# Optimization experiments

Hardware: AMD Instinct MI355X
Metric: run time of the kernel (lower is better)

## Reference

```python
import jax, jax.numpy as jnp
import numpy as np

N = 50000   # nodes
E = 800000  # edges
F = 2       # num_feats
D = 2       # output_dim
H = 64      # hidden_size
L = 2       # num_layers
T = 12      # seq_len
HZN = 12    # horizon
NEG_SLOPE = 0.2


def setup_inputs() -> dict:
    key = jax.random.key(0)
    ks = jax.random.split(key, 10)
    x = jax.random.normal(ks[0], (T, N, F), dtype=jnp.float32)
    src = jax.random.randint(ks[1], (E,), 0, N, dtype=jnp.int32)
    dst = jax.random.randint(ks[2], (E,), 0, N, dtype=jnp.int32)

    def conv_params(k, fin):
        k1, k2, k3 = jax.random.split(k, 3)
        s = 1.0 / np.sqrt(fin)
        W = (jax.random.normal(k1, (3, fin, H), jnp.float32) * s)
        al = (jax.random.normal(k2, (3, H), jnp.float32) * s)
        ar = (jax.random.normal(k3, (3, H), jnp.float32) * s)
        b = jnp.zeros((3, H), jnp.float32)
        return W, al, ar, b

    enc_W0, enc_al0, enc_ar0, enc_b0 = conv_params(ks[3], F + H)
    enc_W1, enc_al1, enc_ar1, enc_b1 = conv_params(ks[4], 2 * H)
    dec_W0, dec_al0, dec_ar0, dec_b0 = conv_params(ks[5], D + H)
    dec_W1, dec_al1, dec_ar1, dec_b1 = conv_params(ks[6], 2 * H)
    proj_W = jax.random.normal(ks[7], (H, D), jnp.float32) / np.sqrt(H)
    proj_b = jnp.zeros((D,), jnp.float32)
    return dict(x=x, src=src, dst=dst,
                enc_W0=enc_W0, enc_al0=enc_al0, enc_ar0=enc_ar0, enc_b0=enc_b0,
                enc_W1=enc_W1, enc_al1=enc_al1, enc_ar1=enc_ar1, enc_b1=enc_b1,
                dec_W0=dec_W0, dec_al0=dec_al0, dec_ar0=dec_ar0, dec_b0=dec_b0,
                dec_W1=dec_W1, dec_al1=dec_al1, dec_ar1=dec_ar1, dec_b1=dec_b1,
                proj_W=proj_W, proj_b=proj_b)


def _gat(feat, W, al, ar, b, src, dst):
    # DGL GATConv, single head: fc -> edge attention -> edge softmax -> aggregate.
    h = feat @ W                              # [N, H]
    el = (h * al).sum(-1)                     # [N] source attention logits
    er = (h * ar).sum(-1)                     # [N] destination attention logits
    e = jax.nn.leaky_relu(el[src] + er[dst], NEG_SLOPE)   # [E]
    m = jax.ops.segment_max(e, dst, num_segments=N)       # per-dst max (stable softmax)
    ex = jnp.exp(e - m[dst])                               # [E]
    s = jax.ops.segment_sum(ex, dst, num_segments=N)       # [N]
    alpha = ex / jnp.maximum(s[dst], 1e-9)                 # [E] edge softmax
    out = jax.ops.segment_sum(h[src] * alpha[:, None], dst, num_segments=N)  # [N, H]
    return out + b


def _gru(xin, hx, W, al, ar, b, src, dst):
    iv = jnp.concatenate([xin, hx], axis=1)
    r = jax.nn.sigmoid(_gat(iv, W[0], al[0], ar[0], b[0], src, dst))
    z = jax.nn.sigmoid(_gat(iv, W[1], al[1], ar[1], b[1], src, dst))
    hc = jnp.tanh(_gat(jnp.concatenate([xin, r * hx], axis=1), W[2], al[2], ar[2], b[2], src, dst))
    return z * hx + (1.0 - z) * hc


def reference(x, src, dst,
              enc_W0, enc_al0, enc_ar0, enc_b0,
              enc_W1, enc_al1, enc_ar1, enc_b1,
              dec_W0, dec_al0, dec_ar0, dec_b0,
              dec_W1, dec_al1, dec_ar1, dec_b1,
              proj_W, proj_b):
    enc_params = [(enc_W0, enc_al0, enc_ar0, enc_b0), (enc_W1, enc_al1, enc_ar1, enc_b1)]
    dec_params = [(dec_W0, dec_al0, dec_ar0, dec_b0), (dec_W1, dec_al1, dec_ar1, dec_b1)]

    def enc_step(hstack, xt):
        out = xt
        new = []
        for i, (W, al, ar, b) in enumerate(enc_params):
            hn = _gru(out, hstack[i], W, al, ar, b, src, dst)
            new.append(hn)
            out = hn
        return jnp.stack(new), None

    h0 = jnp.zeros((L, N, H), x.dtype)
    hT, _ = jax.lax.scan(enc_step, h0, x)

    def dec_step(carry, _):
        dec_in, hstack = carry
        out = dec_in
        new = []
        for i, (W, al, ar, b) in enumerate(dec_params):
            hn = _gru(out, hstack[i], W, al, ar, b, src, dst)
            new.append(hn)
            out = hn
        pred = out @ proj_W + proj_b                 # [N, D]
        return (pred, jnp.stack(new)), pred

    dec_in0 = jnp.zeros((N, D), x.dtype)
    _, outputs = jax.lax.scan(dec_step, (dec_in0, hT), None, length=HZN)
    return outputs  # [horizon, N, output_dim]
```

## Files before the change

kernel.cpp:

```cpp
#include <hip/hip_runtime.h>
#include <hip/hip_bf16.h>

__device__ __forceinline__ float wsum64(float v) {
#pragma unroll
  for (int m = 32; m > 0; m >>= 1) v += __shfl_xor(v, m, 64);
  return v;
}
__device__ __forceinline__ float gsum16(float v) {
#pragma unroll
  for (int m = 8; m > 0; m >>= 1) v += __shfl_xor(v, m, 16);
  return v;
}
__device__ __forceinline__ float lrelu(float x) { return x > 0.f ? x : 0.2f * x; }
__device__ __forceinline__ float sigf(float x) { return 1.f / (1.f + __expf(-x)); }
__device__ __forceinline__ float dp4(float4 a, float4 b) {
  return a.x * b.x + a.y * b.y + a.z * b.z + a.w * b.w;
}

#define MM1(f, row)                                        \
  {                                                        \
    float4 w_ = W4[(row) * 16 + l16];                      \
    acc.x = fmaf((f), w_.x, acc.x);                        \
    acc.y = fmaf((f), w_.y, acc.y);                        \
    acc.z = fmaf((f), w_.z, acc.z);                        \
    acc.w = fmaf((f), w_.w, acc.w);                        \
  }

__global__ void hist_k(const int* __restrict__ dst, int* __restrict__ cnt, int e) {
  int i = blockIdx.x * blockDim.x + threadIdx.x;
  if (i < e) atomicAdd(&cnt[dst[i]], 1);
}

__global__ __launch_bounds__(256) void bsum_k(const int* __restrict__ cnt,
                                              int* __restrict__ bsum, int n) {
  __shared__ int red[4];
  int base = blockIdx.x * 1024;
  int t = threadIdx.x;
  int v = 0;
#pragma unroll
  for (int i = 0; i < 4; i++) {
    int idx = base + t + i * 256;
    v += (idx < n) ? cnt[idx] : 0;
  }
#pragma unroll
  for (int m = 32; m > 0; m >>= 1) v += __shfl_xor(v, m, 64);
  if ((t & 63) == 0) red[t >> 6] = v;
  __syncthreads();
  if (t == 0) bsum[blockIdx.x] = red[0] + red[1] + red[2] + red[3];
}

__global__ __launch_bounds__(1024) void scan_bsum_k(int* __restrict__ bsum,
                                                    int* __restrict__ rpn, int nb) {
  __shared__ int buf[1024];
  int t = threadIdx.x;
  int v = (t < nb) ? bsum[t] : 0;
  buf[t] = v;
  __syncthreads();
  int val = v;
  for (int off = 1; off < 1024; off <<= 1) {
    int u = (t >= off) ? buf[t - off] : 0;
    __syncthreads();
    val += u;
    buf[t] = val;
    __syncthreads();
  }
  if (t < nb) bsum[t] = val - v;
  if (t == nb - 1) *rpn = val;
}

__global__ __launch_bounds__(1024) void scan_fin_k(const int* __restrict__ cnt,
                                                   const int* __restrict__ bsum,
                                                   int* __restrict__ rp,
                                                   int* __restrict__ cursor, int n) {
  __shared__ int buf[1024];
  int t = threadIdx.x;
  int idx = blockIdx.x * 1024 + t;
  int v = (idx < n) ? cnt[idx] : 0;
  buf[t] = v;
  __syncthreads();
  int val = v;
  for (int off = 1; off < 1024; off <<= 1) {
    int u = (t >= off) ? buf[t - off] : 0;
    __syncthreads();
    val += u;
    buf[t] = val;
    __syncthreads();
  }
  if (idx < n) {
    int e = bsum[blockIdx.x] + val - v;
    rp[idx] = e;
    cursor[idx] = e;
  }
}

__global__ void scatter_k(const int* __restrict__ src, const int* __restrict__ dst,
                          int* __restrict__ cursor, int* __restrict__ srcs, int e) {
  int i = blockIdx.x * blockDim.x + threadIdx.x;
  if (i < e) {
    int pos = atomicAdd(&cursor[dst[i]], 1);
    srcs[pos] = src[i];
  }
}

template <int FA>
__global__ __launch_bounds__(512) void mm_k(
    const float* __restrict__ xa, const float* __restrict__ xb,
    const float* __restrict__ Wg, const float* __restrict__ al, const float* __restrict__ ar,
    float* __restrict__ hb, float* __restrict__ el, float* __restrict__ er, int n) {
  constexpr int KP = FA + 64;
  __shared__ float Wl[KP * 128];
  __shared__ float Xl[32 * KP];
  for (int i = threadIdx.x; i < KP * 64; i += 512) {
    float2 wv = {Wg[i], Wg[(size_t)KP * 64 + i]};
    *(float2*)&Wl[i * 2] = wv;
  }
  int rbase = blockIdx.x * 32;
  for (int i = threadIdx.x; i < 32 * KP; i += 512) {
    int row = i / KP, k = i - row * KP;
    int r = rbase + row; if (r >= n) r = n - 1;
    Xl[i] = (k < FA) ? xa[(size_t)r * FA + k] : xb[(size_t)r * 64 + (k - FA)];
  }
  __syncthreads();
  int lane = threadIdx.x & 63, w = threadIdx.x >> 6;
  int rb = rbase + w * 4;
  if (rb >= n) return;
  float alr = al[lane], arr_ = ar[lane];
  float alz = al[64 + lane], arz = ar[64 + lane];
  float accr[4], accz[4];
#pragma unroll
  for (int i = 0; i < 4; i++) { accr[i] = 0.f; accz[i] = 0.f; }
  const int xoff = (w * 4) * KP;
#pragma unroll 8
  for (int k = 0; k < KP; k += 2) {
    float2 w0 = *(const float2*)&Wl[(k * 64 + lane) * 2];
    float2 w1 = *(const float2*)&Wl[((k + 1) * 64 + lane) * 2];
#pragma unroll
    for (int i = 0; i < 4; i++) {
      float2 xv = *(const float2*)&Xl[xoff + i * KP + k];
      accr[i] = fmaf(xv.x, w0.x, accr[i]);
      accz[i] = fmaf(xv.x, w0.y, accz[i]);
      accr[i] = fmaf(xv.y, w1.x, accr[i]);
      accz[i] = fmaf(xv.y, w1.y, accz[i]);
    }
  }
#pragma unroll
  for (int i = 0; i < 4; i++) {
    int r = rb + i;
    bool ok = r < n;
    if (ok) {
      hb[(size_t)r * 128 + lane] = accr[i];
      hb[(size_t)r * 128 + 64 + lane] = accz[i];
    }
    float s0 = wsum64(accr[i] * alr);
    float s1 = wsum64(accz[i] * alz);
    float s2 = wsum64(accr[i] * arr_);
    float s3 = wsum64(accz[i] * arz);
    if (ok && lane == 0) {
      el[(size_t)r * 2 + 0] = s0;
      el[(size_t)r * 2 + 1] = s1;
      er[(size_t)r * 2 + 0] = s2;
      er[(size_t)r * 2 + 1] = s3;
    }
  }
}

template <int FA>
__global__ __launch_bounds__(512) void kb_k(
    const int* __restrict__ rp, const int* __restrict__ srcs,
    const float* __restrict__ hbuf, const float* __restrict__ elrz,
    const float* __restrict__ errz, const float* __restrict__ b,
    const float* __restrict__ xa, const float* __restrict__ hx,
    const float* __restrict__ Wc, const float* __restrict__ alc,
    const float* __restrict__ arc,
    float* __restrict__ hc, float* __restrict__ elc, float* __restrict__ erc,
    float* __restrict__ zb, int n) {
  constexpr int KP = FA + 64;
  __shared__ float WlC[KP * 64];
  for (int i = threadIdx.x; i < KP * 64; i += 512) {
    int k = i >> 6, c = i & 63;
    int ks = (k < 64) ? (FA + k) : (k - 64);
    WlC[i] = Wc[(size_t)ks * 64 + c];
  }
  __syncthreads();
  int l16 = threadIdx.x & 15;
  int d = blockIdx.x * 32 + (threadIdx.x >> 4);
  if (d >= n) return;
  int beg = rp[d], deg = rp[d + 1] - beg;
  float2 erd = ((const float2*)errz)[d];
  const float4* h4 = (const float4*)hbuf;
  float4 accr = {0, 0, 0, 0}, accz = {0, 0, 0, 0};
  float sr = 0.f, sz = 0.f;
  for (int base = 0; base < deg; base += 16) {
    int k = base + l16;
    int s = 0;
    float exr = 0.f, exz = 0.f;
    if (k < deg) {
      s = srcs[beg + k];
      float2 el = ((const float2*)elrz)[s];
      exr = __expf(lrelu(el.x + erd.x));
      exz = __expf(lrelu(el.y + erd.y));
      sr += exr; sz += exz;
    }
#pragma unroll
    for (int j = 0; j < 16; j++) {
      int sj = __shfl(s, j, 16);
      float aj = __shfl(exr, j, 16);
      float zj = __shfl(exz, j, 16);
      float4 hr = h4[(size_t)sj * 32 + l16];
      float4 hz = h4[(size_t)sj * 32 + 16 + l16];
      accr.x = fmaf(aj, hr.x, accr.x); accr.y = fmaf(aj, hr.y, accr.y);
      accr.z = fmaf(aj, hr.z, accr.z); accr.w = fmaf(aj, hr.w, accr.w);
      accz.x = fmaf(zj, hz.x, accz.x); accz.y = fmaf(zj, hz.y, accz.y);
      accz.z = fmaf(zj, hz.z, accz.z); accz.w = fmaf(zj, hz.w, accz.w);
    }
  }
  sr = gsum16(sr); sz = gsum16(sz);
  float invr = 1.f / fmaxf(sr, 1e-9f);
  float invz = 1.f / fmaxf(sz, 1e-9f);
  float4 br4 = ((const float4*)b)[l16];
  float4 bz4 = ((const float4*)(b + 64))[l16];
  float4 hx4 = ((const float4*)hx)[(size_t)d * 16 + l16];
  float4 rv, zv;
  rv.x = sigf(fmaf(accr.x, invr, br4.x)) * hx4.x;
  rv.y = sigf(fmaf(accr.y, invr, br4.y)) * hx4.y;
  rv.z = sigf(fmaf(accr.z, invr, br4.z)) * hx4.z;
  rv.w = sigf(fmaf(accr.w, invr, br4.w)) * hx4.w;
  zv.x = sigf(fmaf(accz.x, invz, bz4.x));
  zv.y = sigf(fmaf(accz.y, invz, bz4.y));
  zv.z = sigf(fmaf(accz.z, invz, bz4.z));
  zv.w = sigf(fmaf(accz.w, invz, bz4.w));
  ((float4*)zb)[(size_t)d * 16 + l16] = zv;
  const float4* W4 = (const float4*)WlC;
  float4 acc = {0, 0, 0, 0};
#pragma unroll
  for (int o = 0; o < 16; o++) {
    float f0 = __shfl(rv.x, o, 16);
    float f1 = __shfl(rv.y, o, 16);
    float f2 = __shfl(rv.z, o, 16);
    float f3 = __shfl(rv.w, o, 16);
    MM1(f0, 4 * o + 0); MM1(f1, 4 * o + 1);
    MM1(f2, 4 * o + 2); MM1(f3, 4 * o + 3);
  }
  if (FA == 2) {
    float f0 = xa[(size_t)d * 2 + 0];
    float f1 = xa[(size_t)d * 2 + 1];
    MM1(f0, 64); MM1(f1, 65);
  } else {
    float4 xv = ((const float4*)xa)[(size_t)d * 16 + l16];
#pragma unroll
    for (int o = 0; o < 16; o++) {
      float f0 = __shfl(xv.x, o, 16);
      float f1 = __shfl(xv.y, o, 16);
      float f2 = __shfl(xv.z, o, 16);
      float f3 = __shfl(xv.w, o, 16);
      MM1(f0, 64 + 4 * o + 0); MM1(f1, 64 + 4 * o + 1);
      MM1(f2, 64 + 4 * o + 2); MM1(f3, 64 + 4 * o + 3);
    }
  }
  float4 alv = ((const float4*)alc)[l16];
  float4 arv = ((const float4*)arc)[l16];
  float sl = gsum16(dp4(acc, alv));
  float sr2 = gsum16(dp4(acc, arv));
  if (l16 == 0) { elc[d] = sl; erc[d] = sr2; }
  ((float4*)hc)[(size_t)d * 16 + l16] = acc;
}

__global__ __launch_bounds__(512) void kc_k(
    const int* __restrict__ rp, const int* __restrict__ srcs,
    const float* __restrict__ hc, const float* __restrict__ elc,
    const float* __restrict__ erc, const float* __restrict__ bc,
    const float* __restrict__ zb, float* __restrict__ hstate,
    const float* __restrict__ projW, const float* __restrict__ projb,
    float* __restrict__ outp, int n) {
  int l16 = threadIdx.x & 15;
  int d = blockIdx.x * 32 + (threadIdx.x >> 4);
  if (d >= n) return;
  int beg = rp[d], deg = rp[d + 1] - beg;
  float erd = erc[d];
  const float4* h4 = (const float4*)hc;
  float4 acg = {0, 0, 0, 0};
  float ssum = 0.f;
  for (int base0 = 0; base0 < deg; base0 += 16) {
    int k = base0 + l16;
    int s = 0;
    float ex = 0.f;
    if (k < deg) {
      s = srcs[beg + k];
      ex = __expf(lrelu(elc[s] + erd));
      ssum += ex;
    }
#pragma unroll
    for (int j = 0; j < 16; j++) {
      int sj = __shfl(s, j, 16);
      float aj = __shfl(ex, j, 16);
      float4 hv = h4[(size_t)sj * 16 + l16];
      acg.x = fmaf(aj, hv.x, acg.x); acg.y = fmaf(aj, hv.y, acg.y);
      acg.z = fmaf(aj, hv.z, acg.z); acg.w = fmaf(aj, hv.w, acg.w);
    }
  }
  ssum = gsum16(ssum);
  float inv = 1.f / fmaxf(ssum, 1e-9f);
  float4 bc4 = ((const float4*)bc)[l16];
  float4 z4 = ((const float4*)zb)[(size_t)d * 16 + l16];
  float4 hx4 = ((const float4*)hstate)[(size_t)d * 16 + l16];
  float4 hcv, hn;
  hcv.x = tanhf(fmaf(acg.x, inv, bc4.x));
  hcv.y = tanhf(fmaf(acg.y, inv, bc4.y));
  hcv.z = tanhf(fmaf(acg.z, inv, bc4.z));
  hcv.w = tanhf(fmaf(acg.w, inv, bc4.w));
  hn.x = z4.x * hx4.x + (1.f - z4.x) * hcv.x;
  hn.y = z4.y * hx4.y + (1.f - z4.y) * hcv.y;
  hn.z = z4.z * hx4.z + (1.f - z4.z) * hcv.z;
  hn.w = z4.w * hx4.w + (1.f - z4.w) * hcv.w;
  ((float4*)hstate)[(size_t)d * 16 + l16] = hn;
  if (outp) {
    const float4* wp4 = (const float4*)projW;
    float4 a0p = wp4[l16 * 2], a1p = wp4[l16 * 2 + 1];
    float p0 = gsum16(hn.x * a0p.x + hn.y * a0p.z + hn.z * a1p.x + hn.w * a1p.z) + projb[0];
    float p1 = gsum16(hn.x * a0p.y + hn.y * a0p.w + hn.z * a1p.y + hn.w * a1p.w) + projb[1];
    if (l16 == 0) {
      outp[(size_t)d * 2 + 0] = p0;
      outp[(size_t)d * 2 + 1] = p1;
    }
  }
}

extern "C" void kernel_launch(void* const* d_in, const int* in_sizes, int n_in,
                              void* d_out, int out_size, void* d_ws, size_t ws_size,
                              hipStream_t stream) {
  const int T = 12, F = 2, H = 64;
  const float* x = (const float*)d_in[0];
  const int* src = (const int*)d_in[1];
  const int* dst = (const int*)d_in[2];
  const float* Ws[4] = {(const float*)d_in[3], (const float*)d_in[7],
                        (const float*)d_in[11], (const float*)d_in[15]};
  const float* als[4] = {(const float*)d_in[4], (const float*)d_in[8],
                         (const float*)d_in[12], (const float*)d_in[16]};
  const float* ars[4] = {(const float*)d_in[5], (const float*)d_in[9],
                         (const float*)d_in[13], (const float*)d_in[17]};
  const float* bs[4] = {(const float*)d_in[6], (const float*)d_in[10],
                        (const float*)d_in[14], (const float*)d_in[18]};
  const float* proj_W = (const float*)d_in[19];
  const float* proj_b = (const float*)d_in[20];
  float* out = (float*)d_out;

  const int E = in_sizes[1];
  const int N = in_sizes[0] / (T * F);
  const int NB = (N + 1023) / 1024;

  char* wp = (char*)d_ws;
  size_t off = 0;
  auto carve = [&](size_t bytes) {
    void* p = wp + off;
    off = (off + bytes + 255) & ~(size_t)255;
    return p;
  };
  int* counts = (int*)carve((size_t)N * 4);
  int* bsum = (int*)carve((size_t)NB * 4);
  int* rp = (int*)carve((size_t)(N + 1) * 4);
  int* cursor = (int*)carve((size_t)N * 4);
  int* srcs = (int*)carve((size_t)E * 4);
  float* hs0 = (float*)carve((size_t)N * H * 4);
  float* hs1 = (float*)carve((size_t)N * H * 4);
  float* hbuf = (float*)carve((size_t)N * 2 * H * 4);
  float* elrz = (float*)carve((size_t)N * 2 * 4);
  float* errz = (float*)carve((size_t)N * 2 * 4);
  float* hcb = (float*)carve((size_t)N * H * 4);
  float* elc = (float*)carve((size_t)N * 4);
  float* erc = (float*)carve((size_t)N * 4);
  float* zbuf = (float*)carve((size_t)N * H * 4);
  float* zero2 = (float*)carve((size_t)N * F * 4);
  (void)ws_size;

  const int G_E = (E + 255) / 256;
  const int G32 = (N + 31) / 32;

  hipMemsetAsync(counts, 0, (size_t)N * 4, stream);
  hist_k<<<G_E, 256, 0, stream>>>(dst, counts, E);
  bsum_k<<<NB, 256, 0, stream>>>(counts, bsum, N);
  scan_bsum_k<<<1, 1024, 0, stream>>>(bsum, rp + N, NB);
  scan_fin_k<<<NB, 1024, 0, stream>>>(counts, bsum, rp, cursor, N);
  scatter_k<<<G_E, 256, 0, stream>>>(src, dst, cursor, srcs, E);

  hipMemsetAsync(hs0, 0, (size_t)N * H * 4, stream);
  hipMemsetAsync(hs1, 0, (size_t)N * H * 4, stream);
  hipMemsetAsync(zero2, 0, (size_t)N * F * 4, stream);

  for (int i = 0; i < 48; i++) {
    bool enc = i < 24;
    int j = enc ? i : i - 24;
    int t = j >> 1, layer = j & 1;
    int type = (enc ? 0 : 2) + layer;
    const float* W = Ws[type];
    const float* al = als[type];
    const float* ar = ars[type];
    const float* b = bs[type];
    int FA = layer ? 64 : 2;
    size_t KP = FA + 64;
    const float* Wc = W + (size_t)2 * KP * 64;
    const float* xa = layer ? hs0
                            : (enc ? x + (size_t)t * N * 2
                                   : (t == 0 ? zero2 : out + (size_t)(t - 1) * N * 2));
    float* hstate = layer ? hs1 : hs0;
    float* outp = (!enc && layer) ? out + (size_t)t * N * 2 : nullptr;

    if (FA == 2) {
      mm_k<2><<<G32, 512, 0, stream>>>(xa, hstate, W, al, ar, hbuf, elrz, errz, N);
      kb_k<2><<<G32, 512, 0, stream>>>(rp, srcs, hbuf, elrz, errz, b, xa, hstate,
                                       Wc, al + 128, ar + 128, hcb, elc, erc, zbuf, N);
    } else {
      mm_k<64><<<G32, 512, 0, stream>>>(xa, hstate, W, al, ar, hbuf, elrz, errz, N);
      kb_k<64><<<G32, 512, 0, stream>>>(rp, srcs, hbuf, elrz, errz, b, xa, hstate,
                                        Wc, al + 128, ar + 128, hcb, elc, erc, zbuf, N);
    }
    kc_k<<<G32, 512, 0, stream>>>(rp, srcs, hcb, elc, erc, b + 128, zbuf, hstate,
                                  proj_W, proj_b, outp, N);
  }
  (void)out_size; (void)n_in;
}
```

Before: 7.665 ms.

## Wavefront-pipeline encoder layers by merging layer-1 step t with layer-0 step t+1

The encoder is reordered so that layer 1 at time t and layer 0 at time t+1 run together. Their attention-aggregation and GRU-update kernels are merged into single launches with twice the grid, and block index picks which cell a block serves. A second set of scratch buffers keeps the two cells' intermediates separate. The goal is fewer serialized launches and more blocks in flight per launch. In exchange, the merged kernels always reserve the larger 128x64 shared tile, and the pipelined path only runs when the workspace is big enough.

```diff
diff --git a/kernel.cpp b/kernel.cpp
--- a/kernel.cpp
+++ b/kernel.cpp
@@ -25,6 +25,16 @@
     acc.z = fmaf((f), w_.z, acc.z);                        \
     acc.w = fmaf((f), w_.w, acc.w);                        \
   }
+
+struct KbArgs {
+  const float* hbuf; const float* elrz; const float* errz; const float* b;
+  const float* xa; const float* hx; const float* Wc; const float* alc; const float* arc;
+  float* hc; float* elc; float* erc; float* zb; int FA;
+};
+struct KcArgs {
+  const float* hc; const float* elc; const float* erc; const float* bc;
+  const float* zb; float* hstate; const float* projW; const float* projb; float* outp;
+};
 
 __global__ void hist_k(const int* __restrict__ dst, int* __restrict__ cnt, int e) {
   int i = blockIdx.x * blockDim.x + threadIdx.x;
@@ -164,30 +174,22 @@
   }
 }
 
-template <int FA>
-__global__ __launch_bounds__(512) void kb_k(
-    const int* __restrict__ rp, const int* __restrict__ srcs,
-    const float* __restrict__ hbuf, const float* __restrict__ elrz,
-    const float* __restrict__ errz, const float* __restrict__ b,
-    const float* __restrict__ xa, const float* __restrict__ hx,
-    const float* __restrict__ Wc, const float* __restrict__ alc,
-    const float* __restrict__ arc,
-    float* __restrict__ hc, float* __restrict__ elc, float* __restrict__ erc,
-    float* __restrict__ zb, int n) {
-  constexpr int KP = FA + 64;
-  __shared__ float WlC[KP * 64];
+__device__ __forceinline__ void kb_core(const int* __restrict__ rp,
+                                        const int* __restrict__ srcs,
+                                        const KbArgs& P, int bid, int n, float* WlC) {
+  const int KP = P.FA + 64;
   for (int i = threadIdx.x; i < KP * 64; i += 512) {
     int k = i >> 6, c = i & 63;
-    int ks = (k < 64) ? (FA + k) : (k - 64);
-    WlC[i] = Wc[(size_t)ks * 64 + c];
+    int ks = (k < 64) ? (P.FA + k) : (k - 64);
+    WlC[i] = P.Wc[(size_t)ks * 64 + c];
   }
   __syncthreads();
   int l16 = threadIdx.x & 15;
-  int d = blockIdx.x * 32 + (threadIdx.x >> 4);
+  int d = bid * 32 + (threadIdx.x >> 4);
   if (d >= n) return;
   int beg = rp[d], deg = rp[d + 1] - beg;
-  float2 erd = ((const float2*)errz)[d];
-  const float4* h4 = (const float4*)hbuf;
+  float2 erd = ((const float2*)P.errz)[d];
+  const float4* h4 = (const float4*)P.hbuf;
   float4 accr = {0, 0, 0, 0}, accz = {0, 0, 0, 0};
   float sr = 0.f, sz = 0.f;
   for (int base = 0; base < deg; base += 16) {
@@ -196,7 +198,7 @@
     float exr = 0.f, exz = 0.f;
     if (k < deg) {
       s = srcs[beg + k];
-      float2 el = ((const float2*)elrz)[s];
+      float2 el = ((const float2*)P.elrz)[s];
       exr = __expf(lrelu(el.x + erd.x));
       exz = __expf(lrelu(el.y + erd.y));
       sr += exr; sz += exz;
@@ -217,9 +219,9 @@
   sr = gsum16(sr); sz = gsum16(sz);
   float invr = 1.f / fmaxf(sr, 1e-9f);
   float invz = 1.f / fmaxf(sz, 1e-9f);
-  float4 br4 = ((const float4*)b)[l16];
-  float4 bz4 = ((const float4*)(b + 64))[l16];
-  float4 hx4 = ((const float4*)hx)[(size_t)d * 16 + l16];
+  float4 br4 = ((const float4*)P.b)[l16];
+  float4 bz4 = ((const float4*)(P.b + 64))[l16];
+  float4 hx4 = ((const float4*)P.hx)[(size_t)d * 16 + l16];
   float4 rv, zv;
   rv.x = sigf(fmaf(accr.x, invr, br4.x)) * hx4.x;
   rv.y = sigf(fmaf(accr.y, invr, br4.y)) * hx4.y;
@@ -229,7 +231,7 @@
   zv.y = sigf(fmaf(accz.y, invz, bz4.y));
   zv.z = sigf(fmaf(accz.z, invz, bz4.z));
   zv.w = sigf(fmaf(accz.w, invz, bz4.w));
-  ((float4*)zb)[(size_t)d * 16 + l16] = zv;
+  ((float4*)P.zb)[(size_t)d * 16 + l16] = zv;
   const float4* W4 = (const float4*)WlC;
   float4 acc = {0, 0, 0, 0};
 #pragma unroll
@@ -241,12 +243,12 @@
     MM1(f0, 4 * o + 0); MM1(f1, 4 * o + 1);
     MM1(f2, 4 * o + 2); MM1(f3, 4 * o + 3);
   }
-  if (FA == 2) {
-    float f0 = xa[(size_t)d * 2 + 0];
-    float f1 = xa[(size_t)d * 2 + 1];
+  if (P.FA == 2) {
+    float f0 = P.xa[(size_t)d * 2 + 0];
+    float f1 = P.xa[(size_t)d * 2 + 1];
     MM1(f0, 64); MM1(f1, 65);
   } else {
-    float4 xv = ((const float4*)xa)[(size_t)d * 16 + l16];
+    float4 xv = ((const float4*)P.xa)[(size_t)d * 16 + l16];
 #pragma unroll
     for (int o = 0; o < 16; o++) {
       float f0 = __shfl(xv.x, o, 16);
@@ -257,27 +259,33 @@
       MM1(f2, 64 + 4 * o + 2); MM1(f3, 64 + 4 * o + 3);
     }
   }
-  float4 alv = ((const float4*)alc)[l16];
-  float4 arv = ((const float4*)arc)[l16];
+  float4 alv = ((const float4*)P.alc)[l16];
+  float4 arv = ((const float4*)P.arc)[l16];
   float sl = gsum16(dp4(acc, alv));
   float sr2 = gsum16(dp4(acc, arv));
-  if (l16 == 0) { elc[d] = sl; erc[d] = sr2; }
-  ((float4*)hc)[(size_t)d * 16 + l16] = acc;
-}
-
-__global__ __launch_bounds__(512) void kc_k(
-    const int* __restrict__ rp, const int* __restrict__ srcs,
-    const float* __restrict__ hc, const float* __restrict__ elc,
-    const float* __restrict__ erc, const float* __restrict__ bc,
-    const float* __restrict__ zb, float* __restrict__ hstate,
-    const float* __restrict__ projW, const float* __restrict__ projb,
-    float* __restrict__ outp, int n) {
+  if (l16 == 0) { P.elc[d] = sl; P.erc[d] = sr2; }
+  ((float4*)P.hc)[(size_t)d * 16 + l16] = acc;
+}
+
+__global__ __launch_bounds__(512) void kbM_k(const int* __restrict__ rp,
+                                             const int* __restrict__ srcs,
+                                             KbArgs A, KbArgs B, int gA, int n) {
+  __shared__ float WlC[128 * 64];
+  bool isA = (int)blockIdx.x < gA;
+  int bid = isA ? blockIdx.x : blockIdx.x - gA;
+  if (isA) kb_core(rp, srcs, A, bid, n, WlC);
+  else     kb_core(rp, srcs, B, bid, n, WlC);
+}
+
+__device__ __forceinline__ void kc_core(const int* __restrict__ rp,
+                                        const int* __restrict__ srcs,
+                                        const KcArgs& P, int bid, int n) {
   int l16 = threadIdx.x & 15;
-  int d = blockIdx.x * 32 + (threadIdx.x >> 4);
+  int d = bid * 32 + (threadIdx.x >> 4);
   if (d >= n) return;
   int beg = rp[d], deg = rp[d + 1] - beg;
-  float erd = erc[d];
-  const float4* h4 = (const float4*)hc;
+  float erd = P.erc[d];
+  const float4* h4 = (const float4*)P.hc;
   float4 acg = {0, 0, 0, 0};
   float ssum = 0.f;
   for (int base0 = 0; base0 < deg; base0 += 16) {
@@ -286,7 +294,7 @@
     float ex = 0.f;
     if (k < deg) {
       s = srcs[beg + k];
-      ex = __expf(lrelu(elc[s] + erd));
+      ex = __expf(lrelu(P.elc[s] + erd));
       ssum += ex;
     }
 #pragma unroll
@@ -300,9 +308,9 @@
   }
   ssum = gsum16(ssum);
   float inv = 1.f / fmaxf(ssum, 1e-9f);
-  float4 bc4 = ((const float4*)bc)[l16];
-  float4 z4 = ((const float4*)zb)[(size_t)d * 16 + l16];
-  float4 hx4 = ((const float4*)hstate)[(size_t)d * 16 + l16];
+  float4 bc4 = ((const float4*)P.bc)[l16];
+  float4 z4 = ((const float4*)P.zb)[(size_t)d * 16 + l16];
+  float4 hx4 = ((const float4*)P.hstate)[(size_t)d * 16 + l16];
   float4 hcv, hn;
   hcv.x = tanhf(fmaf(acg.x, inv, bc4.x));
   hcv.y = tanhf(fmaf(acg.y, inv, bc4.y));
@@ -312,17 +320,26 @@
   hn.y = z4.y * hx4.y + (1.f - z4.y) * hcv.y;
   hn.z = z4.z * hx4.z + (1.f - z4.z) * hcv.z;
   hn.w = z4.w * hx4.w + (1.f - z4.w) * hcv.w;
-  ((float4*)hstate)[(size_t)d * 16 + l16] = hn;
-  if (outp) {
-    const float4* wp4 = (const float4*)projW;
+  ((float4*)P.hstate)[(size_t)d * 16 + l16] = hn;
+  if (P.outp) {
+    const float4* wp4 = (const float4*)P.projW;
     float4 a0p = wp4[l16 * 2], a1p = wp4[l16 * 2 + 1];
-    float p0 = gsum16(hn.x * a0p.x + hn.y * a0p.z + hn.z * a1p.x + hn.w * a1p.z) + projb[0];
-    float p1 = gsum16(hn.x * a0p.y + hn.y * a0p.w + hn.z * a1p.y + hn.w * a1p.w) + projb[1];
+    float p0 = gsum16(hn.x * a0p.x + hn.y * a0p.z + hn.z * a1p.x + hn.w * a1p.z) + P.projb[0];
+    float p1 = gsum16(hn.x * a0p.y + hn.y * a0p.w + hn.z * a1p.y + hn.w * a1p.w) + P.projb[1];
     if (l16 == 0) {
-      outp[(size_t)d * 2 + 0] = p0;
-      outp[(size_t)d * 2 + 1] = p1;
-    }
-  }
+      P.outp[(size_t)d * 2 + 0] = p0;
+      P.outp[(size_t)d * 2 + 1] = p1;
+    }
+  }
+}
+
+__global__ __launch_bounds__(512) void kcM_k(const int* __restrict__ rp,
+                                             const int* __restrict__ srcs,
+                                             KcArgs A, KcArgs B, int gA, int n) {
+  bool isA = (int)blockIdx.x < gA;
+  int bid = isA ? blockIdx.x : blockIdx.x - gA;
+  if (isA) kc_core(rp, srcs, A, bid, n);
+  else     kc_core(rp, srcs, B, bid, n);
 }
 
 extern "C" void kernel_launch(void* const* d_in, const int* in_sizes, int n_in,
@@ -362,15 +379,22 @@
   int* srcs = (int*)carve((size_t)E * 4);
   float* hs0 = (float*)carve((size_t)N * H * 4);
   float* hs1 = (float*)carve((size_t)N * H * 4);
-  float* hbuf = (float*)carve((size_t)N * 2 * H * 4);
-  float* elrz = (float*)carve((size_t)N * 2 * 4);
-  float* errz = (float*)carve((size_t)N * 2 * 4);
-  float* hcb = (float*)carve((size_t)N * H * 4);
-  float* elc = (float*)carve((size_t)N * 4);
-  float* erc = (float*)carve((size_t)N * 4);
-  float* zbuf = (float*)carve((size_t)N * H * 4);
+  float* hbufA = (float*)carve((size_t)N * 2 * H * 4);
+  float* elrzA = (float*)carve((size_t)N * 2 * 4);
+  float* errzA = (float*)carve((size_t)N * 2 * 4);
+  float* hcbA = (float*)carve((size_t)N * H * 4);
+  float* elcA = (float*)carve((size_t)N * 4);
+  float* ercA = (float*)carve((size_t)N * 4);
+  float* zbufA = (float*)carve((size_t)N * H * 4);
   float* zero2 = (float*)carve((size_t)N * F * 4);
-  (void)ws_size;
+  float* hbufB = (float*)carve((size_t)N * 2 * H * 4);
+  float* elrzB = (float*)carve((size_t)N * 2 * 4);
+  float* errzB = (float*)carve((size_t)N * 2 * 4);
+  float* hcbB = (float*)carve((size_t)N * H * 4);
+  float* elcB = (float*)carve((size_t)N * 4);
+  float* ercB = (float*)carve((size_t)N * 4);
+  float* zbufB = (float*)carve((size_t)N * H * 4);
+  const bool pipe = (off <= ws_size);
 
   const int G_E = (E + 255) / 256;
   const int G32 = (N + 31) / 32;
@@ -386,35 +410,66 @@
   hipMemsetAsync(hs1, 0, (size_t)N * H * 4, stream);
   hipMemsetAsync(zero2, 0, (size_t)N * F * 4, stream);
 
-  for (int i = 0; i < 48; i++) {
-    bool enc = i < 24;
-    int j = enc ? i : i - 24;
-    int t = j >> 1, layer = j & 1;
-    int type = (enc ? 0 : 2) + layer;
-    const float* W = Ws[type];
-    const float* al = als[type];
-    const float* ar = ars[type];
-    const float* b = bs[type];
-    int FA = layer ? 64 : 2;
-    size_t KP = FA + 64;
-    const float* Wc = W + (size_t)2 * KP * 64;
-    const float* xa = layer ? hs0
-                            : (enc ? x + (size_t)t * N * 2
-                                   : (t == 0 ? zero2 : out + (size_t)(t - 1) * N * 2));
-    float* hstate = layer ? hs1 : hs0;
-    float* outp = (!enc && layer) ? out + (size_t)t * N * 2 : nullptr;
-
-    if (FA == 2) {
-      mm_k<2><<<G32, 512, 0, stream>>>(xa, hstate, W, al, ar, hbuf, elrz, errz, N);
-      kb_k<2><<<G32, 512, 0, stream>>>(rp, srcs, hbuf, elrz, errz, b, xa, hstate,
-                                       Wc, al + 128, ar + 128, hcb, elc, erc, zbuf, N);
-    } else {
-      mm_k<64><<<G32, 512, 0, stream>>>(xa, hstate, W, al, ar, hbuf, elrz, errz, N);
-      kb_k<64><<<G32, 512, 0, stream>>>(rp, srcs, hbuf, elrz, errz, b, xa, hstate,
-                                        Wc, al + 128, ar + 128, hcb, elc, erc, zbuf, N);
-    }
-    kc_k<<<G32, 512, 0, stream>>>(rp, srcs, hcb, elc, erc, b + 128, zbuf, hstate,
-                                  proj_W, proj_b, outp, N);
+  auto kbArgs = [&](int type, const float* xa, const float* hx, int FA,
+                    float* hbuf, float* elrz, float* errz,
+                    float* hcb, float* elc, float* erc, float* zb) {
+    size_t KP = (size_t)FA + 64;
+    KbArgs a;
+    a.hbuf = hbuf; a.elrz = elrz; a.errz = errz; a.b = bs[type];
+    a.xa = xa; a.hx = hx; a.Wc = Ws[type] + 2 * KP * 64;
+    a.alc = als[type] + 128; a.arc = ars[type] + 128;
+    a.hc = hcb; a.elc = elc; a.erc = erc; a.zb = zb; a.FA = FA;
+    return a;
+  };
+  auto kcArgs = [&](int type, float* hcb, float* elc, float* erc, float* zb,
+                    float* hstate, float* outp) {
+    KcArgs a;
+    a.hc = hcb; a.elc = elc; a.erc = erc; a.bc = bs[type] + 128;
+    a.zb = zb; a.hstate = hstate;
+    a.projW = proj_W; a.projb = proj_b; a.outp = outp;
+    return a;
+  };
+
+  auto run_cell = [&](int type, const float* xa, float* hstate, int FA, float* outp) {
+    if (FA == 2)
+      mm_k<2><<<G32, 512, 0, stream>>>(xa, hstate, Ws[type], als[type], ars[type],
+                                       hbufA, elrzA, errzA, N);
+    else
+      mm_k<64><<<G32, 512, 0, stream>>>(xa, hstate, Ws[type], als[type], ars[type],
+                                        hbufA, elrzA, errzA, N);
+    KbArgs A = kbArgs(type, xa, hstate, FA, hbufA, elrzA, errzA, hcbA, elcA, ercA, zbufA);
+    kbM_k<<<G32, 512, 0, stream>>>(rp, srcs, A, A, G32, N);
+    KcArgs C = kcArgs(type, hcbA, elcA, ercA, zbufA, hstate, outp);
+    kcM_k<<<G32, 512, 0, stream>>>(rp, srcs, C, C, G32, N);
+  };
+
+  if (pipe) {
+    run_cell(0, x, hs0, 2, nullptr);
+    for (int t = 0; t <= 10; t++) {
+      const float* xB = x + (size_t)(t + 1) * N * 2;
+      mm_k<64><<<G32, 512, 0, stream>>>(hs0, hs1, Ws[1], als[1], ars[1],
+                                        hbufA, elrzA, errzA, N);
+      mm_k<2><<<G32, 512, 0, stream>>>(xB, hs0, Ws[0], als[0], ars[0],
+                                       hbufB, elrzB, errzB, N);
+      KbArgs A = kbArgs(1, hs0, hs1, 64, hbufA, elrzA, errzA, hcbA, elcA, ercA, zbufA);
+      KbArgs B = kbArgs(0, xB, hs0, 2, hbufB, elrzB, errzB, hcbB, elcB, ercB, zbufB);
+      kbM_k<<<2 * G32, 512, 0, stream>>>(rp, srcs, A, B, G32, N);
+      KcArgs CA = kcArgs(1, hcbA, elcA, ercA, zbufA, hs1, nullptr);
+      KcArgs CB = kcArgs(0, hcbB, elcB, ercB, zbufB, hs0, nullptr);
+      kcM_k<<<2 * G32, 512, 0, stream>>>(rp, srcs, CA, CB, G32, N);
+    }
+    run_cell(1, hs0, hs1, 64, nullptr);
+  } else {
+    for (int t = 0; t < T; t++) {
+      run_cell(0, x + (size_t)t * N * 2, hs0, 2, nullptr);
+      run_cell(1, hs0, hs1, 64, nullptr);
+    }
+  }
+
+  for (int t = 0; t < T; t++) {
+    const float* xin = (t == 0) ? zero2 : (out + (size_t)(t - 1) * N * 2);
+    run_cell(2, xin, hs0, 2, nullptr);
+    run_cell(3, hs0, hs1, 64, out + (size_t)t * N * 2);
   }
   (void)out_size; (void)n_in;
 }
```

After: 7.674 ms. About the same (+0.1%).
